# Performance work log

Hardware: AMD Instinct MI355X
Metric: run time of the kernel (lower is better)

## Reference

```python
import jax, jax.numpy as jnp
import numpy as np

N = 256        # num_nodes
F = 256        # feature_dim
B = 32         # batch
DEG = 32       # out-degree per node -> E = N*DEG edges


def setup_inputs() -> dict:
    key = jax.random.key(0)
    k1, k2, k3, k4 = jax.random.split(key, 4)
    node_features = jax.random.normal(k1, (B, N, F), dtype=jnp.float32)
    # xavier_uniform for [N, N, F] tensor: fan_in = N*F, fan_out = N*F per torch default flattening
    limit = float(np.sqrt(6.0 / (N * F + N * F)))
    W = jax.random.uniform(k2, (N, N, F), dtype=jnp.float32, minval=-limit, maxval=limit)
    phase = jax.random.uniform(k3, (N, N), dtype=jnp.float32, minval=0.0, maxval=2.0 * np.pi)
    # topology: each node i has DEG outgoing connections (paths[i])
    src = jnp.repeat(jnp.arange(N, dtype=jnp.int64), DEG)              # [E]
    dst = jax.random.randint(k4, (N * DEG,), 0, N, dtype=jnp.int64)    # [E]
    return {"node_features": node_features, "W": W, "phase": phase, "src": src, "dst": dst}


def reference(node_features, W, phase, src, dst):
    # real(exp(i*phase)) == cos(phase); per-edge effective weight [E, F]
    eff_w = W[src, dst, :] * jnp.cos(phase[src, dst])[:, None]
    # gather source node features and scale: [B, E, F]
    signal = node_features[:, src, :] * eff_w[None, :, :]
    # scatter-add into destination nodes
    propagated = jnp.zeros_like(node_features).at[:, dst, :].add(signal)
    # normalization by out-degree of each node index (matches original indexing)
    n = node_features.shape[1]
    counts = jnp.zeros((n,), dtype=node_features.dtype).at[src].add(1.0)
    norm = jnp.maximum(counts, 1.0)
    return propagated / norm[None, :, None]
```

## Files before the change

### kernel.cpp

```cpp
#include <hip/hip_runtime.h>
#include <math.h>

#define NN 256
#define FF 256
#define BB 32
#define EE 8192

#define BGROUPS 2
#define CHUNK 64

__global__ __launch_bounds__(1024) void build_csr_kernel(
    const int* __restrict__ src, const int* __restrict__ dst,
    int* __restrict__ offsets,
    int* __restrict__ edge_ids,
    float* __restrict__ rnorm)
{
    __shared__ int h[NN];
    __shared__ int hs[NN];
    __shared__ int off[NN + 1];
    __shared__ int cur[NN];

    const int tid = threadIdx.x;
    const int nt  = blockDim.x;

    for (int i = tid; i < NN; i += nt) { h[i] = 0; hs[i] = 0; }
    __syncthreads();

    for (int e = tid; e < EE; e += nt) {
        atomicAdd(&h[dst[e]], 1);
        atomicAdd(&hs[src[e]], 1);
    }
    __syncthreads();

    if (tid == 0) {
        int a = 0;
        for (int i = 0; i < NN; i++) { off[i] = a; a += h[i]; }
        off[NN] = a;
    }
    __syncthreads();

    for (int i = tid; i < NN; i += nt) cur[i] = off[i];
    __syncthreads();

    for (int e = tid; e < EE; e += nt) {
        int p = atomicAdd(&cur[dst[e]], 1);
        edge_ids[p] = e;
    }

    for (int i = tid; i < NN + 1; i += nt) offsets[i] = off[i];
    for (int i = tid; i < NN; i += nt)
        rnorm[i] = 1.0f / fmaxf((float)hs[i], 1.0f);
}

__device__ __forceinline__ void fma4(float4& a, const float4 x, const float4 w) {
    a.x = fmaf(x.x, w.x, a.x);
    a.y = fmaf(x.y, w.y, a.y);
    a.z = fmaf(x.z, w.z, a.z);
    a.w = fmaf(x.w, w.w, a.w);
}

__global__ __launch_bounds__(256) void propagate_kernel(
    const float4* __restrict__ nf4,
    const float4* __restrict__ W4,
    const float*  __restrict__ phase,
    const int*    __restrict__ src,
    const int*    __restrict__ offsets,
    const int*    __restrict__ edge_ids,
    const float*  __restrict__ rnorm,
    float4*       __restrict__ out4)
{
    const int d     = blockIdx.x;
    const int b0    = blockIdx.y * (BB / BGROUPS);
    const int tf    = threadIdx.x & 63;
    const int bsub  = threadIdx.x >> 6;
    const int bbase = b0 + bsub * 4;

    __shared__ int   s_s[CHUNK];
    __shared__ float s_c[CHUNK];

    const int beg = offsets[d];
    const int end = offsets[d + 1];

    float4 acc0 = {0.f, 0.f, 0.f, 0.f};
    float4 acc1 = {0.f, 0.f, 0.f, 0.f};
    float4 acc2 = {0.f, 0.f, 0.f, 0.f};
    float4 acc3 = {0.f, 0.f, 0.f, 0.f};

    for (int base = beg; base < end; base += CHUNK) {
        const int m = min(CHUNK, end - base);
        __syncthreads();
        if (threadIdx.x < m) {
            const int e = edge_ids[base + threadIdx.x];
            const int s = src[e];
            s_s[threadIdx.x] = s;
            s_c[threadIdx.x] = cosf(phase[s * NN + d]);
        }
        __syncthreads();

        for (int k = 0; k < m; k++) {
            const int   s = s_s[k];
            const float c = s_c[k];
            float4 w = W4[(s * NN + d) * (FF / 4) + tf];
            w.x *= c; w.y *= c; w.z *= c; w.w *= c;
            const float4 x0 = nf4[((bbase + 0) * NN + s) * (FF / 4) + tf];
            const float4 x1 = nf4[((bbase + 1) * NN + s) * (FF / 4) + tf];
            const float4 x2 = nf4[((bbase + 2) * NN + s) * (FF / 4) + tf];
            const float4 x3 = nf4[((bbase + 3) * NN + s) * (FF / 4) + tf];
            fma4(acc0, x0, w);
            fma4(acc1, x1, w);
            fma4(acc2, x2, w);
            fma4(acc3, x3, w);
        }
    }

    const float rn = rnorm[d];
    float4 o;
    o.x = acc0.x * rn; o.y = acc0.y * rn; o.z = acc0.z * rn; o.w = acc0.w * rn;
    out4[((bbase + 0) * NN + d) * (FF / 4) + tf] = o;
    o.x = acc1.x * rn; o.y = acc1.y * rn; o.z = acc1.z * rn; o.w = acc1.w * rn;
    out4[((bbase + 1) * NN + d) * (FF / 4) + tf] = o;
    o.x = acc2.x * rn; o.y = acc2.y * rn; o.z = acc2.z * rn; o.w = acc2.w * rn;
    out4[((bbase + 2) * NN + d) * (FF / 4) + tf] = o;
    o.x = acc3.x * rn; o.y = acc3.y * rn; o.z = acc3.z * rn; o.w = acc3.w * rn;
    out4[((bbase + 3) * NN + d) * (FF / 4) + tf] = o;
}

extern "C" void kernel_launch(void* const* d_in, const int* in_sizes, int n_in,
                              void* d_out, int out_size, void* d_ws, size_t ws_size,
                              hipStream_t stream) {
    const float* nf    = (const float*)d_in[0];
    const float* W     = (const float*)d_in[1];
    const float* phase = (const float*)d_in[2];
    const int*   src   = (const int*)d_in[3];
    const int*   dst   = (const int*)d_in[4];
    float*       out   = (float*)d_out;

    int*   wsI      = (int*)d_ws;
    int*   offsets  = wsI;
    int*   edge_ids = wsI + 272;
    float* rnorm    = (float*)(wsI + 272 + EE);

    build_csr_kernel<<<1, 1024, 0, stream>>>(src, dst, offsets, edge_ids, rnorm);

    dim3 grid(NN, BGROUPS);
    propagate_kernel<<<grid, 256, 0, stream>>>(
        (const float4*)nf, (const float4*)W, phase, src,
        offsets, edge_ids, rnorm, (float4*)out);
}
```

Before: 134.1 us.

## Fuse CSR build into propagate kernel with per-block edge scan and 4x unroll

Removes the single-block CSR build kernel. Each propagate block now scans all edges itself to collect the sources pointing at its destination node into shared memory, and also counts the out-degree used for normalisation. The accumulation loop is unrolled by four edges so more W and feature loads are in flight at once. The cost is that every block redundantly reads the whole src/dst arrays (8192 edges, 512 times), the list order becomes nondeterministic through shared atomics, and a node with more than 1024 incoming edges would be silently truncated.

```diff
diff --git a/kernel.cpp b/kernel.cpp
--- a/kernel.cpp
+++ b/kernel.cpp
@@ -7,50 +7,7 @@
 #define EE 8192
 
 #define BGROUPS 2
-#define CHUNK 64
-
-__global__ __launch_bounds__(1024) void build_csr_kernel(
-    const int* __restrict__ src, const int* __restrict__ dst,
-    int* __restrict__ offsets,
-    int* __restrict__ edge_ids,
-    float* __restrict__ rnorm)
-{
-    __shared__ int h[NN];
-    __shared__ int hs[NN];
-    __shared__ int off[NN + 1];
-    __shared__ int cur[NN];
-
-    const int tid = threadIdx.x;
-    const int nt  = blockDim.x;
-
-    for (int i = tid; i < NN; i += nt) { h[i] = 0; hs[i] = 0; }
-    __syncthreads();
-
-    for (int e = tid; e < EE; e += nt) {
-        atomicAdd(&h[dst[e]], 1);
-        atomicAdd(&hs[src[e]], 1);
-    }
-    __syncthreads();
-
-    if (tid == 0) {
-        int a = 0;
-        for (int i = 0; i < NN; i++) { off[i] = a; a += h[i]; }
-        off[NN] = a;
-    }
-    __syncthreads();
-
-    for (int i = tid; i < NN; i += nt) cur[i] = off[i];
-    __syncthreads();
-
-    for (int e = tid; e < EE; e += nt) {
-        int p = atomicAdd(&cur[dst[e]], 1);
-        edge_ids[p] = e;
-    }
-
-    for (int i = tid; i < NN + 1; i += nt) offsets[i] = off[i];
-    for (int i = tid; i < NN; i += nt)
-        rnorm[i] = 1.0f / fmaxf((float)hs[i], 1.0f);
-}
+#define CAP 1024
 
 __device__ __forceinline__ void fma4(float4& a, const float4 x, const float4 w) {
     a.x = fmaf(x.x, w.x, a.x);
@@ -59,70 +16,113 @@
     a.w = fmaf(x.w, w.w, a.w);
 }
 
-__global__ __launch_bounds__(256) void propagate_kernel(
+__global__ __launch_bounds__(256) void fused_propagate_kernel(
     const float4* __restrict__ nf4,
     const float4* __restrict__ W4,
     const float*  __restrict__ phase,
     const int*    __restrict__ src,
-    const int*    __restrict__ offsets,
-    const int*    __restrict__ edge_ids,
-    const float*  __restrict__ rnorm,
+    const int*    __restrict__ dst,
     float4*       __restrict__ out4)
 {
     const int d     = blockIdx.x;
-    const int b0    = blockIdx.y * (BB / BGROUPS);
-    const int tf    = threadIdx.x & 63;
-    const int bsub  = threadIdx.x >> 6;
-    const int bbase = b0 + bsub * 4;
+    const int tid   = threadIdx.x;
+    const int tf    = tid & 63;
+    const int bsub  = tid >> 6;
+    const int bbase = blockIdx.y * (BB / BGROUPS) + bsub * 4;
 
-    __shared__ int   s_s[CHUNK];
-    __shared__ float s_c[CHUNK];
+    __shared__ int   ls[CAP];
+    __shared__ float lc[CAP];
+    __shared__ int   s_cnt;
+    __shared__ int   s_srccnt;
+    __shared__ int   s_n;
 
-    const int beg = offsets[d];
-    const int end = offsets[d + 1];
+    if (tid == 0) { s_cnt = 0; s_srccnt = 0; }
+    __syncthreads();
+
+    const int4* dst4 = (const int4*)dst;
+    const int4* src4 = (const int4*)src;
+    int mysrc = 0;
+    for (int i = tid; i < EE / 4; i += 256) {
+        const int4 dv = dst4[i];
+        const int4 sv = src4[i];
+        if (dv.x == d) { int p = atomicAdd(&s_cnt, 1); if (p < CAP) { ls[p] = sv.x; lc[p] = cosf(phase[sv.x * NN + d]); } }
+        if (dv.y == d) { int p = atomicAdd(&s_cnt, 1); if (p < CAP) { ls[p] = sv.y; lc[p] = cosf(phase[sv.y * NN + d]); } }
+        if (dv.z == d) { int p = atomicAdd(&s_cnt, 1); if (p < CAP) { ls[p] = sv.z; lc[p] = cosf(phase[sv.z * NN + d]); } }
+        if (dv.w == d) { int p = atomicAdd(&s_cnt, 1); if (p < CAP) { ls[p] = sv.w; lc[p] = cosf(phase[sv.w * NN + d]); } }
+        mysrc += (sv.x == d) + (sv.y == d) + (sv.z == d) + (sv.w == d);
+    }
+    if (mysrc) atomicAdd(&s_srccnt, mysrc);
+    __syncthreads();
+
+    if (tid == 0) {
+        int n  = min(s_cnt, CAP);
+        int n4 = (n + 3) & ~3;
+        for (int i = n; i < n4; i++) { ls[i] = 0; lc[i] = 0.0f; }
+        s_n = n4;
+    }
+    __syncthreads();
+
+    const int   nlist = s_n;
+    const float rn    = 1.0f / fmaxf((float)s_srccnt, 1.0f);
 
     float4 acc0 = {0.f, 0.f, 0.f, 0.f};
     float4 acc1 = {0.f, 0.f, 0.f, 0.f};
     float4 acc2 = {0.f, 0.f, 0.f, 0.f};
     float4 acc3 = {0.f, 0.f, 0.f, 0.f};
 
-    for (int base = beg; base < end; base += CHUNK) {
-        const int m = min(CHUNK, end - base);
-        __syncthreads();
-        if (threadIdx.x < m) {
-            const int e = edge_ids[base + threadIdx.x];
-            const int s = src[e];
-            s_s[threadIdx.x] = s;
-            s_c[threadIdx.x] = cosf(phase[s * NN + d]);
-        }
-        __syncthreads();
+    const int woff = d * (FF / 4) + tf;
+    const int nfo0 = (bbase + 0) * NN * (FF / 4) + tf;
+    const int nfo1 = (bbase + 1) * NN * (FF / 4) + tf;
+    const int nfo2 = (bbase + 2) * NN * (FF / 4) + tf;
+    const int nfo3 = (bbase + 3) * NN * (FF / 4) + tf;
 
-        for (int k = 0; k < m; k++) {
-            const int   s = s_s[k];
-            const float c = s_c[k];
-            float4 w = W4[(s * NN + d) * (FF / 4) + tf];
-            w.x *= c; w.y *= c; w.z *= c; w.w *= c;
-            const float4 x0 = nf4[((bbase + 0) * NN + s) * (FF / 4) + tf];
-            const float4 x1 = nf4[((bbase + 1) * NN + s) * (FF / 4) + tf];
-            const float4 x2 = nf4[((bbase + 2) * NN + s) * (FF / 4) + tf];
-            const float4 x3 = nf4[((bbase + 3) * NN + s) * (FF / 4) + tf];
-            fma4(acc0, x0, w);
-            fma4(acc1, x1, w);
-            fma4(acc2, x2, w);
-            fma4(acc3, x3, w);
-        }
+    for (int k = 0; k < nlist; k += 4) {
+        const int   s0 = ls[k + 0], s1 = ls[k + 1], s2 = ls[k + 2], s3 = ls[k + 3];
+        const float c0 = lc[k + 0], c1 = lc[k + 1], c2 = lc[k + 2], c3 = lc[k + 3];
+
+        float4 w0 = W4[s0 * (NN * FF / 4) + woff];
+        float4 w1 = W4[s1 * (NN * FF / 4) + woff];
+        float4 w2 = W4[s2 * (NN * FF / 4) + woff];
+        float4 w3 = W4[s3 * (NN * FF / 4) + woff];
+
+        const float4 x00 = nf4[nfo0 + s0 * (FF / 4)];
+        const float4 x01 = nf4[nfo1 + s0 * (FF / 4)];
+        const float4 x02 = nf4[nfo2 + s0 * (FF / 4)];
+        const float4 x03 = nf4[nfo3 + s0 * (FF / 4)];
+        const float4 x10 = nf4[nfo0 + s1 * (FF / 4)];
+        const float4 x11 = nf4[nfo1 + s1 * (FF / 4)];
+        const float4 x12 = nf4[nfo2 + s1 * (FF / 4)];
+        const float4 x13 = nf4[nfo3 + s1 * (FF / 4)];
+        const float4 x20 = nf4[nfo0 + s2 * (FF / 4)];
+        const float4 x21 = nf4[nfo1 + s2 * (FF / 4)];
+        const float4 x22 = nf4[nfo2 + s2 * (FF / 4)];
+        const float4 x23 = nf4[nfo3 + s2 * (FF / 4)];
+        const float4 x30 = nf4[nfo0 + s3 * (FF / 4)];
+        const float4 x31 = nf4[nfo1 + s3 * (FF / 4)];
+        const float4 x32 = nf4[nfo2 + s3 * (FF / 4)];
+        const float4 x33 = nf4[nfo3 + s3 * (FF / 4)];
+
+        w0.x *= c0; w0.y *= c0; w0.z *= c0; w0.w *= c0;
+        w1.x *= c1; w1.y *= c1; w1.z *= c1; w1.w *= c1;
+        w2.x *= c2; w2.y *= c2; w2.z *= c2; w2.w *= c2;
+        w3.x *= c3; w3.y *= c3; w3.z *= c3; w3.w *= c3;
+
+        fma4(acc0, x00, w0); fma4(acc1, x01, w0); fma4(acc2, x02, w0); fma4(acc3, x03, w0);
+        fma4(acc0, x10, w1); fma4(acc1, x11, w1); fma4(acc2, x12, w1); fma4(acc3, x13, w1);
+        fma4(acc0, x20, w2); fma4(acc1, x21, w2); fma4(acc2, x22, w2); fma4(acc3, x23, w2);
+        fma4(acc0, x30, w3); fma4(acc1, x31, w3); fma4(acc2, x32, w3); fma4(acc3, x33, w3);
     }
 
-    const float rn = rnorm[d];
+    const int oo = d * (FF / 4) + tf;
     float4 o;
     o.x = acc0.x * rn; o.y = acc0.y * rn; o.z = acc0.z * rn; o.w = acc0.w * rn;
-    out4[((bbase + 0) * NN + d) * (FF / 4) + tf] = o;
+    out4[(bbase + 0) * NN * (FF / 4) + oo] = o;
     o.x = acc1.x * rn; o.y = acc1.y * rn; o.z = acc1.z * rn; o.w = acc1.w * rn;
-    out4[((bbase + 1) * NN + d) * (FF / 4) + tf] = o;
+    out4[(bbase + 1) * NN * (FF / 4) + oo] = o;
     o.x = acc2.x * rn; o.y = acc2.y * rn; o.z = acc2.z * rn; o.w = acc2.w * rn;
-    out4[((bbase + 2) * NN + d) * (FF / 4) + tf] = o;
+    out4[(bbase + 2) * NN * (FF / 4) + oo] = o;
     o.x = acc3.x * rn; o.y = acc3.y * rn; o.z = acc3.z * rn; o.w = acc3.w * rn;
-    out4[((bbase + 3) * NN + d) * (FF / 4) + tf] = o;
+    out4[(bbase + 3) * NN * (FF / 4) + oo] = o;
 }
 
 extern "C" void kernel_launch(void* const* d_in, const int* in_sizes, int n_in,
@@ -135,15 +135,7 @@
     const int*   dst   = (const int*)d_in[4];
     float*       out   = (float*)d_out;
 
-    int*   wsI      = (int*)d_ws;
-    int*   offsets  = wsI;
-    int*   edge_ids = wsI + 272;
-    float* rnorm    = (float*)(wsI + 272 + EE);
-
-    build_csr_kernel<<<1, 1024, 0, stream>>>(src, dst, offsets, edge_ids, rnorm);
-
     dim3 grid(NN, BGROUPS);
-    propagate_kernel<<<grid, 256, 0, stream>>>(
-        (const float4*)nf, (const float4*)W, phase, src,
-        offsets, edge_ids, rnorm, (float4*)out);
+    fused_propagate_kernel<<<grid, 256, 0, stream>>>(
+        (const float4*)nf, (const float4*)W, phase, src, dst, (float4*)out);
 }
```

After: 127.7 us. 1.05x faster.
